# Kernel tuning notes

Hardware: AMD Instinct MI355X
Metric: run time of the kernel (lower is better)

The kernel has to match this reference:

```python
import jax, jax.numpy as jnp
import numpy as np

N, E, G = 100000, 1600000, 64
IN_DIM, EMB, HID, HEADS, OUT = 128, 128, 32, 4, 64
CAT = HID * HEADS  # 128
EPS = 1e-5
SLOPE = 0.2


def gat_conv(x, src, dst, W, a_src, a_dst, bias):
    # x: [N, F_in]; W: [HEADS*HID, F_in]; a_*: [1, HEADS, HID]; bias: [HEADS*HID]
    h = (x @ W.T).reshape(N, HEADS, HID)
    s_src = (h * a_src).sum(-1)  # [N, HEADS]
    s_dst = (h * a_dst).sum(-1)
    e = jax.nn.leaky_relu(s_src[src] + s_dst[dst], SLOPE)  # [Etot, HEADS]
    m = jax.ops.segment_max(e, dst, num_segments=N)
    p = jnp.exp(e - m[dst])
    denom = jax.ops.segment_sum(p, dst, num_segments=N)
    alpha = p / denom[dst]  # softmax over incoming edges per dst node
    out = jax.ops.segment_sum(h[src] * alpha[:, :, None], dst, num_segments=N)
    return out.reshape(N, CAT) + bias


def graph_norm(x, batch, w, b, mean_scale):
    cnt = jax.ops.segment_sum(jnp.ones((N,), x.dtype), batch, num_segments=G)[:, None]
    mean = jax.ops.segment_sum(x, batch, num_segments=G) / cnt  # [G, C]
    sub = x - mean_scale * mean[batch]
    var = jax.ops.segment_sum(sub * sub, batch, num_segments=G) / cnt
    inv = 1.0 / jnp.sqrt(var + EPS)
    return w * sub * inv[batch] + b


def setup_inputs() -> dict:
    key = jax.random.key(0)
    ks = jax.random.split(key, 20)
    g = lambda k, shape, s: jax.random.normal(k, shape, dtype=jnp.float32) * s
    inp = {
        'x': g(ks[0], (N, IN_DIM), 1.0),
        'edge_index': jax.random.randint(ks[1], (2, E), 0, N, dtype=jnp.int64 if jax.config.read('jax_enable_x64') else jnp.int32),
        'batch': jnp.sort(jax.random.randint(ks[2], (N,), 0, G)),
        'enc_w': g(ks[3], (EMB, IN_DIM), 0.08),
        'enc_b': jnp.zeros((EMB,), jnp.float32),
        'w1': g(ks[4], (HEADS * HID, EMB), 0.08),
        'att_src1': g(ks[5], (1, HEADS, HID), 0.15),
        'att_dst1': g(ks[6], (1, HEADS, HID), 0.15),
        'b1': jnp.zeros((CAT,), jnp.float32),
        'n1_w': jnp.ones((CAT,), jnp.float32),
        'n1_b': jnp.zeros((CAT,), jnp.float32),
        'n1_ms': jnp.ones((CAT,), jnp.float32),
        'w2': g(ks[7], (HEADS * HID, CAT), 0.08),
        'att_src2': g(ks[8], (1, HEADS, HID), 0.15),
        'att_dst2': g(ks[9], (1, HEADS, HID), 0.15),
        'b2': jnp.zeros((CAT,), jnp.float32),
        'n2_w': jnp.ones((CAT,), jnp.float32),
        'n2_b': jnp.zeros((CAT,), jnp.float32),
        'n2_ms': jnp.ones((CAT,), jnp.float32),
        'fc_w': g(ks[10], (OUT, CAT), 0.08),
        'fc_b': jnp.zeros((OUT,), jnp.float32),
    }
    return inp


def reference(x, edge_index, batch, enc_w, enc_b, w1, att_src1, att_dst1, b1,
              n1_w, n1_b, n1_ms, w2, att_src2, att_dst2, b2, n2_w, n2_b, n2_ms,
              fc_w, fc_b):
    # PyG GATConv adds self-loops by default
    loops = jnp.arange(N, dtype=edge_index.dtype)
    src = jnp.concatenate([edge_index[0], loops])
    dst = jnp.concatenate([edge_index[1], loops])

    h = x @ enc_w.T + enc_b
    h = jax.nn.elu(gat_conv(h, src, dst, w1, att_src1, att_dst1, b1))
    h = graph_norm(h, batch, n1_w, n1_b, n1_ms)  # dropout = identity (eval)
    h = jax.nn.elu(gat_conv(h, src, dst, w2, att_src2, att_dst2, b2))
    h = graph_norm(h, batch, n2_w, n2_b, n2_ms)
    pooled = jax.ops.segment_max(h, batch, num_segments=G)  # global_max_pool
    return pooled @ fc_w.T + fc_b  # out_dim != 1 -> no sigmoid
```

## Files before the change

kernel.cpp:

```cpp
#include <hip/hip_runtime.h>
#include <hip/hip_bf16.h>

#define SLOPE 0.2f
#define EPS_GN 1e-5f
#define APITCH 136
#define NBUCK 391

typedef __attribute__((ext_vector_type(8))) short bfrag;
typedef __attribute__((ext_vector_type(4))) float ffrag;

__device__ __forceinline__ float lrelu(float v) { return v > 0.f ? v : SLOPE * v; }
__device__ __forceinline__ short f2bs(float v) {
    __hip_bfloat16 h = __float2bfloat16(v);
    return *reinterpret_cast<short*>(&h);
}
__device__ __forceinline__ float blo(unsigned int u) { return __uint_as_float(u << 16); }
__device__ __forceinline__ float bhi(unsigned int u) { return __uint_as_float(u & 0xffff0000u); }

__global__ void prep_weights(const float* __restrict__ enc_w,
                             const float* __restrict__ enc_b,
                             const float* __restrict__ w1,
                             const float* __restrict__ w2,
                             unsigned short* __restrict__ WT1b,
                             unsigned short* __restrict__ WT2b,
                             float* __restrict__ bc1, float* __restrict__ bc2) {
    int c = blockIdx.x;
    int k = threadIdx.x;
    __shared__ float w1row[128];
    w1row[k] = w1[c * 128 + k];
    __syncthreads();
    float acc = 0.f;
    for (int j = 0; j < 128; ++j)
        acc = fmaf(w1row[j], enc_w[j * 128 + k], acc);
    WT1b[c * 128 + k] = (unsigned short)f2bs(acc);
    WT2b[c * 128 + k] = (unsigned short)f2bs(w2[c * 128 + k]);
    if (k == 0) {
        float b = 0.f;
        for (int j = 0; j < 128; ++j) b += w1row[j] * enc_b[j];
        bc1[c] = b;
        bc2[c] = 0.f;
    }
}


__global__ void __launch_bounds__(256) bucket_hist(const int* __restrict__ ei,
                                                   int* __restrict__ bhist, int E, int N) {
    __shared__ int h[NBUCK];
    for (int i = threadIdx.x; i < NBUCK; i += 256) h[i] = 0;
    __syncthreads();
    int base = blockIdx.x * 4096;
#pragma unroll
    for (int s = 0; s < 16; ++s) {
        int e = base + s * 256 + threadIdx.x;
        if (e < E + N) {
            int dst = (e < E) ? ei[E + e] : (e - E);
            atomicAdd(&h[dst >> 8], 1);
        }
    }
    __syncthreads();
    for (int i = threadIdx.x; i < NBUCK; i += 256)
        if (h[i]) atomicAdd(&bhist[i], h[i]);
}

__global__ void bucket_scan(const int* __restrict__ bhist,
                            int* __restrict__ bbase, int* __restrict__ bcur) {
    __shared__ int sh[512];
    int t = threadIdx.x;
    int v = (t < NBUCK) ? bhist[t] : 0;
    sh[t] = v;
    __syncthreads();
    for (int off = 1; off < 512; off <<= 1) {
        int add = (t >= off) ? sh[t - off] : 0;
        __syncthreads();
        sh[t] += add;
        __syncthreads();
    }
    if (t < NBUCK) {
        bbase[t] = sh[t] - v;
        bcur[t] = sh[t] - v;
    }
}

__global__ void __launch_bounds__(256) bucket_scatter(const int* __restrict__ ei,
                                                      int* __restrict__ bcur,
                                                      unsigned int* __restrict__ staging,
                                                      int E, int N) {
    __shared__ int h[NBUCK];
    __shared__ int lb[NBUCK];
    for (int i = threadIdx.x; i < NBUCK; i += 256) h[i] = 0;
    __syncthreads();
    int base = blockIdx.x * 4096;
    int srcv[16], dstv[16];
#pragma unroll
    for (int s = 0; s < 16; ++s) {
        int e = base + s * 256 + threadIdx.x;
        srcv[s] = -1;
        if (e < E + N) {
            srcv[s] = (e < E) ? ei[e] : (e - E);
            dstv[s] = (e < E) ? ei[E + e] : (e - E);
            atomicAdd(&h[dstv[s] >> 8], 1);
        }
    }
    __syncthreads();
    for (int i = threadIdx.x; i < NBUCK; i += 256) {
        int c = h[i];
        lb[i] = c ? atomicAdd(&bcur[i], c) : 0;
        h[i] = 0;
    }
    __syncthreads();
#pragma unroll
    for (int s = 0; s < 16; ++s) {
        if (srcv[s] >= 0) {
            int b = dstv[s] >> 8;
            int slot = atomicAdd(&h[b], 1);
            staging[lb[b] + slot] = ((unsigned int)srcv[s] << 8) | (unsigned int)(dstv[s] & 255);
        }
    }
}

__global__ void __launch_bounds__(256) bucket_finalize(
    const unsigned int* __restrict__ staging,
    const int* __restrict__ bbase, const int* __restrict__ bcur,
    int* __restrict__ rowp, int* __restrict__ esrc, int N, int Etot) {
    int b = blockIdx.x, t = threadIdx.x;
    __shared__ int h[256], sc[256];
    h[t] = 0;
    __syncthreads();
    int s0 = bbase[b], s1 = bcur[b];
    for (int j = s0 + t; j < s1; j += 256)
        atomicAdd(&h[staging[j] & 255], 1);
    __syncthreads();
    int d = h[t];
    sc[t] = d;
    __syncthreads();
    for (int off = 1; off < 256; off <<= 1) {
        int add = (t >= off) ? sc[t - off] : 0;
        __syncthreads();
        sc[t] += add;
        __syncthreads();
    }
    int excl = s0 + sc[t] - d;
    int node = b * 256 + t;
    if (node < N) rowp[node] = excl;
    if (b == 0 && t == 0) rowp[N] = Etot;
    __syncthreads();
    h[t] = excl;
    __syncthreads();
    for (int j = s0 + t; j < s1; j += 256) {
        unsigned int p = staging[j];
        int pos = atomicAdd(&h[p & 255], 1);
        esrc[pos] = (int)(p >> 8);
    }
}

__global__ void __launch_bounds__(256) gemm_mfma(
    const void* __restrict__ Ain, const unsigned short* __restrict__ WTb,
    const float* __restrict__ bias, const float* __restrict__ att_src,
    const float* __restrict__ att_dst, const int* __restrict__ batch,
    const float* __restrict__ Ac, const float* __restrict__ Bc,
    unsigned int* __restrict__ H, float* __restrict__ ssrc, float* __restrict__ sdst, int N) {
    __shared__ short Bsh[128 * APITCH];
    __shared__ short Ash[64 * APITCH];
    __shared__ float asrc_s[128], adst_s[128], bias_s[128];
    int tid = threadIdx.x;
    int base = blockIdx.x * 64;

    for (int idx = tid; idx < 2048; idx += 256) {
        int c = idx >> 4, k8 = (idx & 15) * 8;
        uint4 wv = ((const uint4*)WTb)[idx];
        *(uint4*)&Bsh[c * APITCH + k8] = wv;
    }
    if (Ac == nullptr) {
        const float* A = (const float*)Ain;
        for (int idx = tid; idx < 2048; idx += 256) {
            int nl = idx >> 5, k4 = (idx & 31) * 4;
            int node = base + nl;
            float4 v = make_float4(0.f, 0.f, 0.f, 0.f);
            if (node < N) v = ((const float4*)A)[node * 32 + (idx & 31)];
            *(short4*)&Ash[nl * APITCH + k4] =
                make_short4(f2bs(v.x), f2bs(v.y), f2bs(v.z), f2bs(v.w));
        }
    } else {
        const uint4* A4 = (const uint4*)Ain;
        for (int idx = tid; idx < 1024; idx += 256) {
            int nl = idx >> 4, u4 = idx & 15, k8 = u4 * 8;
            int node = base + nl;
            short o[8] = {0, 0, 0, 0, 0, 0, 0, 0};
            if (node < N) {
                uint4 hb = A4[node * 16 + u4];
                int g = batch[node];
                float4 a0 = *(const float4*)&Ac[g * 128 + k8];
                float4 a1 = *(const float4*)&Ac[g * 128 + k8 + 4];
                float4 b0 = *(const float4*)&Bc[g * 128 + k8];
                float4 b1 = *(const float4*)&Bc[g * 128 + k8 + 4];
                o[0] = f2bs(fmaf(blo(hb.x), a0.x, b0.x));
                o[1] = f2bs(fmaf(bhi(hb.x), a0.y, b0.y));
                o[2] = f2bs(fmaf(blo(hb.y), a0.z, b0.z));
                o[3] = f2bs(fmaf(bhi(hb.y), a0.w, b0.w));
                o[4] = f2bs(fmaf(blo(hb.z), a1.x, b1.x));
                o[5] = f2bs(fmaf(bhi(hb.z), a1.y, b1.y));
                o[6] = f2bs(fmaf(blo(hb.w), a1.z, b1.z));
                o[7] = f2bs(fmaf(bhi(hb.w), a1.w, b1.w));
            }
            *(bfrag*)&Ash[nl * APITCH + k8] = *(bfrag*)o;
        }
    }
    if (tid < 128) {
        asrc_s[tid] = att_src[tid];
        adst_s[tid] = att_dst[tid];
        bias_s[tid] = bias[tid];
    }
    __syncthreads();

    int w = tid >> 6, lane = tid & 63, col = lane & 15, quad = lane >> 4;
    int rowBase = w * 16;

    bfrag afr[4];
#pragma unroll
    for (int s = 0; s < 4; ++s)
        afr[s] = *(const bfrag*)&Ash[(rowBase + col) * APITCH + s * 32 + quad * 8];

    ffrag acc[8];
#pragma unroll
    for (int t = 0; t < 8; ++t) acc[t] = (ffrag){0.f, 0.f, 0.f, 0.f};

#pragma unroll
    for (int t = 0; t < 8; ++t) {
#pragma unroll
        for (int s = 0; s < 4; ++s) {
            bfrag bfr = *(const bfrag*)&Bsh[(t * 16 + col) * APITCH + s * 32 + quad * 8];
            acc[t] = __builtin_amdgcn_mfma_f32_16x16x32_bf16(afr[s], bfr, acc[t], 0, 0, 0);
        }
    }

#pragma unroll
    for (int t = 0; t < 8; ++t) {
        int ch = t * 16 + col;
        float bv = bias_s[ch];
#pragma unroll
        for (int r = 0; r < 4; ++r)
            Ash[(rowBase + quad * 4 + r) * APITCH + ch] = f2bs(acc[t][r] + bv);
    }
    __syncthreads();

    float2 av = make_float2(asrc_s[lane * 2], asrc_s[lane * 2 + 1]);
    float2 dv = make_float2(adst_s[lane * 2], adst_s[lane * 2 + 1]);
    for (int r = 0; r < 16; ++r) {
        int node = base + rowBase + r;
        unsigned int hb = *(const unsigned int*)&Ash[(rowBase + r) * APITCH + lane * 2];
        float hx = blo(hb);
        float hy = bhi(hb);
        float vs = hx * av.x + hy * av.y;
        float vd = hx * dv.x + hy * dv.y;
#pragma unroll
        for (int off = 8; off; off >>= 1) {
            vs += __shfl_xor(vs, off, 16);
            vd += __shfl_xor(vd, off, 16);
        }
        if (node < N) {
            H[node * 64 + lane] = hb;
            if ((lane & 15) == 0) {
                int h = lane >> 4;
                ssrc[node * 4 + h] = vs;
                sdst[node * 4 + h] = vd;
            }
        }
    }
}

__global__ void __launch_bounds__(256) agg_kernel(
    const int* __restrict__ row, const int* __restrict__ esrc,
    const float* __restrict__ ssrc, const float* __restrict__ sdst,
    const uint4* __restrict__ H4, const float* __restrict__ bias,
    uint4* __restrict__ out, int N) {
    int n = (blockIdx.x * 256 + threadIdx.x) >> 6;
    int lane = threadIdx.x & 63;
    if (n >= N) return;
    int slot = lane >> 4, li = lane & 15, head = li >> 2;
    int beg = row[n], end = row[n + 1];
    float sdh = sdst[n * 4 + head];

    float num[8] = {0.f, 0.f, 0.f, 0.f, 0.f, 0.f, 0.f, 0.f};
    float den = 0.f;
    for (int e = beg + slot; e < end; e += 4) {
        int s = esrc[e];
        float al = __expf(lrelu(ssrc[s * 4 + head] + sdh));
        uint4 hb = H4[s * 16 + li];
        den += al;
        num[0] = fmaf(al, blo(hb.x), num[0]);
        num[1] = fmaf(al, bhi(hb.x), num[1]);
        num[2] = fmaf(al, blo(hb.y), num[2]);
        num[3] = fmaf(al, bhi(hb.y), num[3]);
        num[4] = fmaf(al, blo(hb.z), num[4]);
        num[5] = fmaf(al, bhi(hb.z), num[5]);
        num[6] = fmaf(al, blo(hb.w), num[6]);
        num[7] = fmaf(al, bhi(hb.w), num[7]);
    }
    den += __shfl_xor(den, 16);
    den += __shfl_xor(den, 32);
#pragma unroll
    for (int j = 0; j < 8; ++j) {
        num[j] += __shfl_xor(num[j], 16);
        num[j] += __shfl_xor(num[j], 32);
    }
    if (slot == 0) {
        float rh = 1.f / den;
        int c0 = li * 8;
        unsigned int o[4];
#pragma unroll
        for (int p = 0; p < 4; ++p) {
            float v0 = fmaf(num[2 * p], rh, bias[c0 + 2 * p]);
            float v1 = fmaf(num[2 * p + 1], rh, bias[c0 + 2 * p + 1]);
            v0 = v0 > 0.f ? v0 : __expf(v0) - 1.f;
            v1 = v1 > 0.f ? v1 : __expf(v1) - 1.f;
            o[p] = ((unsigned int)(unsigned short)f2bs(v0)) |
                   (((unsigned int)(unsigned short)f2bs(v1)) << 16);
        }
        out[n * 16 + li] = make_uint4(o[0], o[1], o[2], o[3]);
    }
}

template <int POOL>
__global__ void __launch_bounds__(256) stats_kernel(
    const uint4* __restrict__ X4, const int* __restrict__ batch,
    float* __restrict__ part, int N) {
    __shared__ float red[16][16][9];
    int t = threadIdx.x, u4 = t & 15, rg = t >> 4;
    int base = blockIdx.x * 64;
    int g0 = batch[base];

    float s[2][8] = {}, q[2][8] = {};
    float mx[2][8], mn[2][8];
#pragma unroll
    for (int st = 0; st < 2; ++st)
#pragma unroll
        for (int p = 0; p < 8; ++p) { mx[st][p] = -3e38f; mn[st][p] = 3e38f; }

#pragma unroll
    for (int rr = 0; rr < 4; ++rr) {
        int node = base + rg + rr * 16;
        if (node < N) {
            uint4 hb = X4[node * 16 + u4];
            int st = (batch[node] != g0) ? 1 : 0;
            float vv[8] = {blo(hb.x), bhi(hb.x), blo(hb.y), bhi(hb.y),
                           blo(hb.z), bhi(hb.z), blo(hb.w), bhi(hb.w)};
#pragma unroll
            for (int p = 0; p < 8; ++p) {
                s[st][p] += vv[p];
                q[st][p] += vv[p] * vv[p];
                if (POOL) {
                    mx[st][p] = fmaxf(mx[st][p], vv[p]);
                    mn[st][p] = fminf(mn[st][p], vv[p]);
                }
            }
        }
    }

    int uu = t >> 3, ch = t & 7;
    float rs[2] = {0.f, 0.f}, rq[2] = {0.f, 0.f};
    float rmx[2] = {-3e38f, -3e38f}, rmn[2] = {3e38f, 3e38f};
    for (int st = 0; st < 2; ++st) {
#pragma unroll
        for (int p = 0; p < 8; ++p) red[rg][u4][p] = s[st][p];
        __syncthreads();
        if (t < 128) { float a = 0.f; for (int r2 = 0; r2 < 16; ++r2) a += red[r2][uu][ch]; rs[st] = a; }
        __syncthreads();
#pragma unroll
        for (int p = 0; p < 8; ++p) red[rg][u4][p] = q[st][p];
        __syncthreads();
        if (t < 128) { float a = 0.f; for (int r2 = 0; r2 < 16; ++r2) a += red[r2][uu][ch]; rq[st] = a; }
        __syncthreads();
        if (POOL) {
#pragma unroll
            for (int p = 0; p < 8; ++p) red[rg][u4][p] = mx[st][p];
            __syncthreads();
            if (t < 128) { float a = -3e38f; for (int r2 = 0; r2 < 16; ++r2) a = fmaxf(a, red[r2][uu][ch]); rmx[st] = a; }
            __syncthreads();
#pragma unroll
            for (int p = 0; p < 8; ++p) red[rg][u4][p] = mn[st][p];
            __syncthreads();
            if (t < 128) { float a = 3e38f; for (int r2 = 0; r2 < 16; ++r2) a = fminf(a, red[r2][uu][ch]); rmn[st] = a; }
            __syncthreads();
        }
    }
    if (t < 128) {
        float* pb = part + (size_t)blockIdx.x * 8 * 128;
        pb[0 * 128 + t] = rs[0];
        pb[1 * 128 + t] = rq[0];
        pb[2 * 128 + t] = rs[1];
        pb[3 * 128 + t] = rq[1];
        if (POOL) {
            pb[4 * 128 + t] = rmx[0];
            pb[5 * 128 + t] = rmn[0];
            pb[6 * 128 + t] = rmx[1];
            pb[7 * 128 + t] = rmn[1];
        }
    }
}

template <int POOL>
__global__ void reduce_coef(const float* __restrict__ part,
                            const int* __restrict__ batch, int N,
                            const float* __restrict__ w, const float* __restrict__ b,
                            const float* __restrict__ ms,
                            float* __restrict__ Ac, float* __restrict__ Bc,
                            float* __restrict__ pooled) {
    __shared__ int sh2[2];
    int g = blockIdx.x, c = threadIdx.x;
    if (c < 2) {
        int key = g + c;
        int lo = 0, hi = N;
        while (lo < hi) { int m = (lo + hi) >> 1; if (batch[m] < key) lo = m + 1; else hi = m; }
        sh2[c] = lo;
    }
    __syncthreads();
    int sidx = sh2[0], eidx = sh2[1];
    float cnt = (float)(eidx - sidx);
    if (cnt < 0.5f) {
        if (POOL) pooled[g * 128 + c] = 0.f;
        else { Ac[g * 128 + c] = 0.f; Bc[g * 128 + c] = 0.f; }
        return;
    }
    int b0 = sidx >> 6, b1 = (eidx - 1) >> 6;
    float s = 0.f, q = 0.f, M = -3e38f, m = 3e38f;
    for (int bb = b0; bb <= b1; ++bb) {
        int g0b = batch[bb << 6];
        int qoff;
        bool take;
        if (g0b == g) { qoff = 0; take = true; }
        else {
            int g1b = batch[min((bb << 6) + 63, N - 1)];
            take = (g1b == g);
            qoff = 2;
        }
        if (take) {
            const float* pb = part + (size_t)bb * 8 * 128;
            s += pb[qoff * 128 + c];
            q += pb[(qoff + 1) * 128 + c];
            if (POOL) {
                M = fmaxf(M, pb[(4 + qoff) * 128 + c]);
                m = fminf(m, pb[(5 + qoff) * 128 + c]);
            }
        }
    }
    float mean = s / cnt;
    float msv = ms[c];
    float var = q / cnt - msv * (2.f - msv) * mean * mean;
    var = fmaxf(var, 0.f);
    float inv = rsqrtf(var + EPS_GN);
    float a = w[c] * inv;
    float bb2 = b[c] - msv * mean * a;
    if (POOL) pooled[g * 128 + c] = (a >= 0.f) ? fmaf(a, M, bb2) : fmaf(a, m, bb2);
    else { Ac[g * 128 + c] = a; Bc[g * 128 + c] = bb2; }
}

__global__ void fc_kernel(const float* __restrict__ pooled,
                          const float* __restrict__ fcw,
                          const float* __restrict__ fcb,
                          float* __restrict__ out) {
    int g = blockIdx.x, o = threadIdx.x;
    __shared__ float p[128];
    p[o] = pooled[g * 128 + o];
    p[o + 64] = pooled[g * 128 + 64 + o];
    __syncthreads();
    float acc = fcb[o];
    for (int k = 0; k < 128; ++k)
        acc = fmaf(p[k], fcw[o * 128 + k], acc);
    out[g * 64 + o] = acc;
}

extern "C" void kernel_launch(void* const* d_in, const int* in_sizes, int n_in,
                              void* d_out, int out_size, void* d_ws, size_t ws_size,
                              hipStream_t stream) {
    const float* x     = (const float*)d_in[0];
    const int* ei      = (const int*)d_in[1];
    const int* batch   = (const int*)d_in[2];
    const float* enc_w = (const float*)d_in[3];
    const float* enc_b = (const float*)d_in[4];
    const float* w1    = (const float*)d_in[5];
    const float* as1   = (const float*)d_in[6];
    const float* ad1   = (const float*)d_in[7];
    const float* b1    = (const float*)d_in[8];
    const float* n1w   = (const float*)d_in[9];
    const float* n1b   = (const float*)d_in[10];
    const float* n1ms  = (const float*)d_in[11];
    const float* w2    = (const float*)d_in[12];
    const float* as2   = (const float*)d_in[13];
    const float* ad2   = (const float*)d_in[14];
    const float* b2    = (const float*)d_in[15];
    const float* n2w   = (const float*)d_in[16];
    const float* n2b   = (const float*)d_in[17];
    const float* n2ms  = (const float*)d_in[18];
    const float* fcw   = (const float*)d_in[19];
    const float* fcb   = (const float*)d_in[20];
    float* out = (float*)d_out;

    int N = in_sizes[2];
    int E = in_sizes[1] / 2;
    int Etot = E + N;
    int SB = (N + 63) / 64;

    char* ws = (char*)d_ws;
    size_t off = 0;
    auto take = [&](size_t bytes) {
        char* p = ws + off;
        off = (off + bytes + 255) & ~(size_t)255;
        return p;
    };
    unsigned short* WT1b = (unsigned short*)take(128 * 128 * 2);
    unsigned short* WT2b = (unsigned short*)take(128 * 128 * 2);
    float* bc1 = (float*)take(512);
    float* bc2 = (float*)take(512);
    float* ssrc = (float*)take((size_t)N * 16);
    float* sdst = (float*)take((size_t)N * 16);
    int* rowp   = (int*)take((size_t)(N + 1) * 4);
    int* esrc   = (int*)take((size_t)Etot * 4);
    unsigned int* staging = (unsigned int*)take((size_t)Etot * 4);
    int* bbase  = (int*)take(512 * 4);
    int* bcur   = (int*)take(512 * 4);
    int* bhist  = (int*)take(512 * 4);
    unsigned int* H = (unsigned int*)take((size_t)N * 256);
    unsigned int* AG = (unsigned int*)take((size_t)N * 256);
    float* Ac   = (float*)take(64 * 128 * 4);
    float* Bc   = (float*)take(64 * 128 * 4);
    float* part = (float*)take((size_t)SB * 8 * 128 * 4);
    float* pooled = (float*)take(64 * 128 * 4);
    if (off > ws_size) return;

    int EB = (Etot + 4095) / 4096;

    hipMemsetAsync(bhist, 0, 512 * 4, stream);
    prep_weights<<<128, 128, 0, stream>>>(enc_w, enc_b, w1, w2, WT1b, WT2b, bc1, bc2);

    bucket_hist<<<EB, 256, 0, stream>>>(ei, bhist, E, N);
    bucket_scan<<<1, 512, 0, stream>>>(bhist, bbase, bcur);
    bucket_scatter<<<EB, 256, 0, stream>>>(ei, bcur, staging, E, N);
    bucket_finalize<<<NBUCK, 256, 0, stream>>>(staging, bbase, bcur, rowp, esrc, N, Etot);

    gemm_mfma<<<(N + 63) / 64, 256, 0, stream>>>(x, WT1b, bc1, as1, ad1, batch,
                                                 nullptr, nullptr, H, ssrc, sdst, N);
    agg_kernel<<<(N + 3) / 4, 256, 0, stream>>>(rowp, esrc, ssrc, sdst,
                                                (const uint4*)H, b1, (uint4*)AG, N);
    stats_kernel<0><<<SB, 256, 0, stream>>>((const uint4*)AG, batch, part, N);
    reduce_coef<0><<<64, 128, 0, stream>>>(part, batch, N, n1w, n1b, n1ms, Ac, Bc, nullptr);

    gemm_mfma<<<(N + 63) / 64, 256, 0, stream>>>(AG, WT2b, bc2, as2, ad2, batch,
                                                 Ac, Bc, H, ssrc, sdst, N);
    agg_kernel<<<(N + 3) / 4, 256, 0, stream>>>(rowp, esrc, ssrc, sdst,
                                                (const uint4*)H, b2, (uint4*)AG, N);
    stats_kernel<1><<<SB, 256, 0, stream>>>((const uint4*)AG, batch, part, N);
    reduce_coef<1><<<64, 128, 0, stream>>>(part, batch, N, n2w, n2b, n2ms,
                                           nullptr, nullptr, pooled);

    fc_kernel<<<64, 64, 0, stream>>>(pooled, fcw, fcb, out);
}
```

Before: 468.5 us.

## Fuse setup kernels, load GEMM operands directly to registers, merge final reduce with FC

Merges weight preparation and the bucket histogram into one launch, and merges the second graph-norm reduction with the final FC layer. The GEMM kernel now loads its A fragments straight from global memory into registers and reads B fragments from global memory, with no shared-memory staging, which shrinks LDS use and removes a barrier. The intent is fewer kernel launches and less LDS traffic, at the cost of repeated global (L2) reads of the weight matrix by every wave.

```diff
diff --git a/kernel.cpp b/kernel.cpp
--- a/kernel.cpp
+++ b/kernel.cpp
@@ -17,50 +17,51 @@
 __device__ __forceinline__ float blo(unsigned int u) { return __uint_as_float(u << 16); }
 __device__ __forceinline__ float bhi(unsigned int u) { return __uint_as_float(u & 0xffff0000u); }
 
-__global__ void prep_weights(const float* __restrict__ enc_w,
-                             const float* __restrict__ enc_b,
-                             const float* __restrict__ w1,
-                             const float* __restrict__ w2,
-                             unsigned short* __restrict__ WT1b,
-                             unsigned short* __restrict__ WT2b,
-                             float* __restrict__ bc1, float* __restrict__ bc2) {
-    int c = blockIdx.x;
-    int k = threadIdx.x;
-    __shared__ float w1row[128];
-    w1row[k] = w1[c * 128 + k];
-    __syncthreads();
-    float acc = 0.f;
-    for (int j = 0; j < 128; ++j)
-        acc = fmaf(w1row[j], enc_w[j * 128 + k], acc);
-    WT1b[c * 128 + k] = (unsigned short)f2bs(acc);
-    WT2b[c * 128 + k] = (unsigned short)f2bs(w2[c * 128 + k]);
-    if (k == 0) {
-        float b = 0.f;
-        for (int j = 0; j < 128; ++j) b += w1row[j] * enc_b[j];
-        bc1[c] = b;
-        bc2[c] = 0.f;
-    }
-}
-
-
-__global__ void __launch_bounds__(256) bucket_hist(const int* __restrict__ ei,
-                                                   int* __restrict__ bhist, int E, int N) {
-    __shared__ int h[NBUCK];
-    for (int i = threadIdx.x; i < NBUCK; i += 256) h[i] = 0;
-    __syncthreads();
-    int base = blockIdx.x * 4096;
-#pragma unroll
-    for (int s = 0; s < 16; ++s) {
-        int e = base + s * 256 + threadIdx.x;
-        if (e < E + N) {
-            int dst = (e < E) ? ei[E + e] : (e - E);
-            atomicAdd(&h[dst >> 8], 1);
-        }
-    }
-    __syncthreads();
-    for (int i = threadIdx.x; i < NBUCK; i += 256)
-        if (h[i]) atomicAdd(&bhist[i], h[i]);
-}
+__global__ void __launch_bounds__(256) setup_kernel(
+    const int* __restrict__ ei, int* __restrict__ bhist, int E, int N, int EB,
+    const float* __restrict__ enc_w, const float* __restrict__ enc_b,
+    const float* __restrict__ w1, const float* __restrict__ w2,
+    unsigned short* __restrict__ WT1b, unsigned short* __restrict__ WT2b,
+    float* __restrict__ bc1, float* __restrict__ bc2) {
+    __shared__ int shmem[NBUCK];
+    int tid = threadIdx.x;
+    if ((int)blockIdx.x < EB) {
+        for (int i = tid; i < NBUCK; i += 256) shmem[i] = 0;
+        __syncthreads();
+        int base = blockIdx.x * 4096;
+#pragma unroll
+        for (int s = 0; s < 16; ++s) {
+            int e = base + s * 256 + tid;
+            if (e < E + N) {
+                int dst = (e < E) ? ei[E + e] : (e - E);
+                atomicAdd(&shmem[dst >> 8], 1);
+            }
+        }
+        __syncthreads();
+        for (int i = tid; i < NBUCK; i += 256)
+            if (shmem[i]) atomicAdd(&bhist[i], shmem[i]);
+    } else {
+        int c = blockIdx.x - EB;
+        float* w1row = (float*)shmem;
+        if (tid < 128) w1row[tid] = w1[c * 128 + tid];
+        __syncthreads();
+        if (tid < 128) {
+            int k = tid;
+            float acc = 0.f;
+            for (int j = 0; j < 128; ++j)
+                acc = fmaf(w1row[j], enc_w[j * 128 + k], acc);
+            WT1b[c * 128 + k] = (unsigned short)f2bs(acc);
+            WT2b[c * 128 + k] = (unsigned short)f2bs(w2[c * 128 + k]);
+            if (k == 0) {
+                float b = 0.f;
+                for (int j = 0; j < 128; ++j) b += w1row[j] * enc_b[j];
+                bc1[c] = b;
+                bc2[c] = 0.f;
+            }
+        }
+    }
+}
+
 
 __global__ void bucket_scan(const int* __restrict__ bhist,
                             int* __restrict__ bbase, int* __restrict__ bcur) {
@@ -159,36 +160,45 @@
     const float* __restrict__ att_dst, const int* __restrict__ batch,
     const float* __restrict__ Ac, const float* __restrict__ Bc,
     unsigned int* __restrict__ H, float* __restrict__ ssrc, float* __restrict__ sdst, int N) {
-    __shared__ short Bsh[128 * APITCH];
-    __shared__ short Ash[64 * APITCH];
+    __shared__ short Csh[64 * APITCH];
     __shared__ float asrc_s[128], adst_s[128], bias_s[128];
     int tid = threadIdx.x;
     int base = blockIdx.x * 64;
-
-    for (int idx = tid; idx < 2048; idx += 256) {
-        int c = idx >> 4, k8 = (idx & 15) * 8;
-        uint4 wv = ((const uint4*)WTb)[idx];
-        *(uint4*)&Bsh[c * APITCH + k8] = wv;
-    }
+    if (tid < 128) {
+        asrc_s[tid] = att_src[tid];
+        adst_s[tid] = att_dst[tid];
+        bias_s[tid] = bias[tid];
+    }
+
+    int w = tid >> 6, lane = tid & 63, col = lane & 15, quad = lane >> 4;
+    int rowBase = w * 16;
+    int node = base + rowBase + col;
+    bool valid = node < N;
+
+    bfrag afr[4];
     if (Ac == nullptr) {
         const float* A = (const float*)Ain;
-        for (int idx = tid; idx < 2048; idx += 256) {
-            int nl = idx >> 5, k4 = (idx & 31) * 4;
-            int node = base + nl;
-            float4 v = make_float4(0.f, 0.f, 0.f, 0.f);
-            if (node < N) v = ((const float4*)A)[node * 32 + (idx & 31)];
-            *(short4*)&Ash[nl * APITCH + k4] =
-                make_short4(f2bs(v.x), f2bs(v.y), f2bs(v.z), f2bs(v.w));
+#pragma unroll
+        for (int s = 0; s < 4; ++s) {
+            short o[8] = {0, 0, 0, 0, 0, 0, 0, 0};
+            if (valid) {
+                int k8 = s * 32 + quad * 8;
+                float4 v0 = *(const float4*)&A[(size_t)node * 128 + k8];
+                float4 v1 = *(const float4*)&A[(size_t)node * 128 + k8 + 4];
+                o[0] = f2bs(v0.x); o[1] = f2bs(v0.y); o[2] = f2bs(v0.z); o[3] = f2bs(v0.w);
+                o[4] = f2bs(v1.x); o[5] = f2bs(v1.y); o[6] = f2bs(v1.z); o[7] = f2bs(v1.w);
+            }
+            afr[s] = *(bfrag*)o;
         }
     } else {
         const uint4* A4 = (const uint4*)Ain;
-        for (int idx = tid; idx < 1024; idx += 256) {
-            int nl = idx >> 4, u4 = idx & 15, k8 = u4 * 8;
-            int node = base + nl;
+        int g = valid ? batch[node] : 0;
+#pragma unroll
+        for (int s = 0; s < 4; ++s) {
             short o[8] = {0, 0, 0, 0, 0, 0, 0, 0};
-            if (node < N) {
-                uint4 hb = A4[node * 16 + u4];
-                int g = batch[node];
+            if (valid) {
+                int k8 = s * 32 + quad * 8;
+                uint4 hb = A4[(size_t)node * 16 + s * 4 + quad];
                 float4 a0 = *(const float4*)&Ac[g * 128 + k8];
                 float4 a1 = *(const float4*)&Ac[g * 128 + k8 + 4];
                 float4 b0 = *(const float4*)&Bc[g * 128 + k8];
@@ -202,23 +212,9 @@
                 o[6] = f2bs(fmaf(blo(hb.w), a1.z, b1.z));
                 o[7] = f2bs(fmaf(bhi(hb.w), a1.w, b1.w));
             }
-            *(bfrag*)&Ash[nl * APITCH + k8] = *(bfrag*)o;
-        }
-    }
-    if (tid < 128) {
-        asrc_s[tid] = att_src[tid];
-        adst_s[tid] = att_dst[tid];
-        bias_s[tid] = bias[tid];
-    }
-    __syncthreads();
-
-    int w = tid >> 6, lane = tid & 63, col = lane & 15, quad = lane >> 4;
-    int rowBase = w * 16;
-
-    bfrag afr[4];
-#pragma unroll
-    for (int s = 0; s < 4; ++s)
-        afr[s] = *(const bfrag*)&Ash[(rowBase + col) * APITCH + s * 32 + quad * 8];
+            afr[s] = *(bfrag*)o;
+        }
+    }
 
     ffrag acc[8];
 #pragma unroll
@@ -228,26 +224,27 @@
     for (int t = 0; t < 8; ++t) {
 #pragma unroll
         for (int s = 0; s < 4; ++s) {
-            bfrag bfr = *(const bfrag*)&Bsh[(t * 16 + col) * APITCH + s * 32 + quad * 8];
+            bfrag bfr = *(const bfrag*)&WTb[(t * 16 + col) * 128 + s * 32 + quad * 8];
             acc[t] = __builtin_amdgcn_mfma_f32_16x16x32_bf16(afr[s], bfr, acc[t], 0, 0, 0);
         }
     }
 
+    __syncthreads();
 #pragma unroll
     for (int t = 0; t < 8; ++t) {
         int ch = t * 16 + col;
         float bv = bias_s[ch];
 #pragma unroll
         for (int r = 0; r < 4; ++r)
-            Ash[(rowBase + quad * 4 + r) * APITCH + ch] = f2bs(acc[t][r] + bv);
+            Csh[(rowBase + quad * 4 + r) * APITCH + ch] = f2bs(acc[t][r] + bv);
     }
     __syncthreads();
 
     float2 av = make_float2(asrc_s[lane * 2], asrc_s[lane * 2 + 1]);
     float2 dv = make_float2(adst_s[lane * 2], adst_s[lane * 2 + 1]);
     for (int r = 0; r < 16; ++r) {
-        int node = base + rowBase + r;
-        unsigned int hb = *(const unsigned int*)&Ash[(rowBase + r) * APITCH + lane * 2];
+        int n2 = base + rowBase + r;
+        unsigned int hb = *(const unsigned int*)&Csh[(rowBase + r) * APITCH + lane * 2];
         float hx = blo(hb);
         float hy = bhi(hb);
         float vs = hx * av.x + hy * av.y;
@@ -257,12 +254,12 @@
             vs += __shfl_xor(vs, off, 16);
             vd += __shfl_xor(vd, off, 16);
         }
-        if (node < N) {
-            H[node * 64 + lane] = hb;
+        if (n2 < N) {
+            H[n2 * 64 + lane] = hb;
             if ((lane & 15) == 0) {
                 int h = lane >> 4;
-                ssrc[node * 4 + h] = vs;
-                sdst[node * 4 + h] = vd;
+                ssrc[n2 * 4 + h] = vs;
+                sdst[n2 * 4 + h] = vd;
             }
         }
     }
@@ -398,13 +395,11 @@
     }
 }
 
-template <int POOL>
 __global__ void reduce_coef(const float* __restrict__ part,
                             const int* __restrict__ batch, int N,
                             const float* __restrict__ w, const float* __restrict__ b,
                             const float* __restrict__ ms,
-                            float* __restrict__ Ac, float* __restrict__ Bc,
-                            float* __restrict__ pooled) {
+                            float* __restrict__ Ac, float* __restrict__ Bc) {
     __shared__ int sh2[2];
     int g = blockIdx.x, c = threadIdx.x;
     if (c < 2) {
@@ -416,13 +411,9 @@
     __syncthreads();
     int sidx = sh2[0], eidx = sh2[1];
     float cnt = (float)(eidx - sidx);
-    if (cnt < 0.5f) {
-        if (POOL) pooled[g * 128 + c] = 0.f;
-        else { Ac[g * 128 + c] = 0.f; Bc[g * 128 + c] = 0.f; }
-        return;
-    }
+    if (cnt < 0.5f) { Ac[g * 128 + c] = 0.f; Bc[g * 128 + c] = 0.f; return; }
     int b0 = sidx >> 6, b1 = (eidx - 1) >> 6;
-    float s = 0.f, q = 0.f, M = -3e38f, m = 3e38f;
+    float s = 0.f, q = 0.f;
     for (int bb = b0; bb <= b1; ++bb) {
         int g0b = batch[bb << 6];
         int qoff;
@@ -437,10 +428,6 @@
             const float* pb = part + (size_t)bb * 8 * 128;
             s += pb[qoff * 128 + c];
             q += pb[(qoff + 1) * 128 + c];
-            if (POOL) {
-                M = fmaxf(M, pb[(4 + qoff) * 128 + c]);
-                m = fminf(m, pb[(5 + qoff) * 128 + c]);
-            }
         }
     }
     float mean = s / cnt;
@@ -449,24 +436,67 @@
     var = fmaxf(var, 0.f);
     float inv = rsqrtf(var + EPS_GN);
     float a = w[c] * inv;
-    float bb2 = b[c] - msv * mean * a;
-    if (POOL) pooled[g * 128 + c] = (a >= 0.f) ? fmaf(a, M, bb2) : fmaf(a, m, bb2);
-    else { Ac[g * 128 + c] = a; Bc[g * 128 + c] = bb2; }
-}
-
-__global__ void fc_kernel(const float* __restrict__ pooled,
-                          const float* __restrict__ fcw,
-                          const float* __restrict__ fcb,
-                          float* __restrict__ out) {
-    int g = blockIdx.x, o = threadIdx.x;
+    Ac[g * 128 + c] = a;
+    Bc[g * 128 + c] = b[c] - msv * mean * a;
+}
+
+__global__ void __launch_bounds__(128) reduce_fc(
+    const float* __restrict__ part, const int* __restrict__ batch, int N,
+    const float* __restrict__ w, const float* __restrict__ b,
+    const float* __restrict__ ms,
+    const float* __restrict__ fcw, const float* __restrict__ fcb,
+    float* __restrict__ out) {
+    __shared__ int sh2[2];
     __shared__ float p[128];
-    p[o] = pooled[g * 128 + o];
-    p[o + 64] = pooled[g * 128 + 64 + o];
-    __syncthreads();
-    float acc = fcb[o];
-    for (int k = 0; k < 128; ++k)
-        acc = fmaf(p[k], fcw[o * 128 + k], acc);
-    out[g * 64 + o] = acc;
+    int g = blockIdx.x, c = threadIdx.x;
+    if (c < 2) {
+        int key = g + c;
+        int lo = 0, hi = N;
+        while (lo < hi) { int m = (lo + hi) >> 1; if (batch[m] < key) lo = m + 1; else hi = m; }
+        sh2[c] = lo;
+    }
+    __syncthreads();
+    int sidx = sh2[0], eidx = sh2[1];
+    float cnt = (float)(eidx - sidx);
+    if (cnt < 0.5f) {
+        p[c] = 0.f;
+    } else {
+        int b0 = sidx >> 6, b1 = (eidx - 1) >> 6;
+        float s = 0.f, q = 0.f, M = -3e38f, m = 3e38f;
+        for (int bb = b0; bb <= b1; ++bb) {
+            int g0b = batch[bb << 6];
+            int qoff;
+            bool take;
+            if (g0b == g) { qoff = 0; take = true; }
+            else {
+                int g1b = batch[min((bb << 6) + 63, N - 1)];
+                take = (g1b == g);
+                qoff = 2;
+            }
+            if (take) {
+                const float* pb = part + (size_t)bb * 8 * 128;
+                s += pb[qoff * 128 + c];
+                q += pb[(qoff + 1) * 128 + c];
+                M = fmaxf(M, pb[(4 + qoff) * 128 + c]);
+                m = fminf(m, pb[(5 + qoff) * 128 + c]);
+            }
+        }
+        float mean = s / cnt;
+        float msv = ms[c];
+        float var = q / cnt - msv * (2.f - msv) * mean * mean;
+        var = fmaxf(var, 0.f);
+        float inv = rsqrtf(var + EPS_GN);
+        float a = w[c] * inv;
+        float bb2 = b[c] - msv * mean * a;
+        p[c] = (a >= 0.f) ? fmaf(a, M, bb2) : fmaf(a, m, bb2);
+    }
+    __syncthreads();
+    if (c < 64) {
+        float acc = fcb[c];
+        for (int k = 0; k < 128; ++k)
+            acc = fmaf(p[k], fcw[c * 128 + k], acc);
+        out[g * 64 + c] = acc;
+    }
 }
 
 extern "C" void kernel_launch(void* const* d_in, const int* in_sizes, int n_in,
@@ -499,6 +529,7 @@
     int E = in_sizes[1] / 2;
     int Etot = E + N;
     int SB = (N + 63) / 64;
+    int EB = (Etot + 4095) / 4096;
 
     char* ws = (char*)d_ws;
     size_t off = 0;
@@ -524,15 +555,12 @@
     float* Ac   = (float*)take(64 * 128 * 4);
     float* Bc   = (float*)take(64 * 128 * 4);
     float* part = (float*)take((size_t)SB * 8 * 128 * 4);
-    float* pooled = (float*)take(64 * 128 * 4);
     if (off > ws_size) return;
 
-    int EB = (Etot + 4095) / 4096;
-
     hipMemsetAsync(bhist, 0, 512 * 4, stream);
-    prep_weights<<<128, 128, 0, stream>>>(enc_w, enc_b, w1, w2, WT1b, WT2b, bc1, bc2);
-
-    bucket_hist<<<EB, 256, 0, stream>>>(ei, bhist, E, N);
+    setup_kernel<<<EB + 128, 256, 0, stream>>>(ei, bhist, E, N, EB,
+                                               enc_w, enc_b, w1, w2,
+                                               WT1b, WT2b, bc1, bc2);
     bucket_scan<<<1, 512, 0, stream>>>(bhist, bbase, bcur);
     bucket_scatter<<<EB, 256, 0, stream>>>(ei, bcur, staging, E, N);
     bucket_finalize<<<NBUCK, 256, 0, stream>>>(staging, bbase, bcur, rowp, esrc, N, Etot);
@@ -542,15 +570,12 @@
     agg_kernel<<<(N + 3) / 4, 256, 0, stream>>>(rowp, esrc, ssrc, sdst,
                                                 (const uint4*)H, b1, (uint4*)AG, N);
     stats_kernel<0><<<SB, 256, 0, stream>>>((const uint4*)AG, batch, part, N);
-    reduce_coef<0><<<64, 128, 0, stream>>>(part, batch, N, n1w, n1b, n1ms, Ac, Bc, nullptr);
+    reduce_coef<<<64, 128, 0, stream>>>(part, batch, N, n1w, n1b, n1ms, Ac, Bc);
 
     gemm_mfma<<<(N + 63) / 64, 256, 0, stream>>>(AG, WT2b, bc2, as2, ad2, batch,
                                                  Ac, Bc, H, ssrc, sdst, N);
     agg_kernel<<<(N + 3) / 4, 256, 0, stream>>>(rowp, esrc, ssrc, sdst,
                                                 (const uint4*)H, b2, (uint4*)AG, N);
     stats_kernel<1><<<SB, 256, 0, stream>>>((const uint4*)AG, batch, part, N);
-    reduce_coef<1><<<64, 128, 0, stream>>>(part, batch, N, n2w, n2b, n2ms,
-                                           nullptr, nullptr, pooled);
-
-    fc_kernel<<<64, 64, 0, stream>>>(pooled, fcw, fcb, out);
-}
+    reduce_fc<<<64, 128, 0, stream>>>(part, batch, N, n2w, n2b, n2ms, fcw, fcb, out);
+}
```

Measured after the change: 473.8 us. No clear change (+1.1%).
